# Kernel optimization log

Hardware: AMD Instinct MI355X
Metric: run time of the kernel (lower is better)

Reference implementation:

```python
import jax, jax.numpy as jnp
import numpy as np
from jax import lax

H = 32      # n_heads
D = 128     # head_dim
HID = 4096  # hidden_dim
CQ, CK, CH = 4, 9, 2
G = H // CH  # conv groups == groupnorm groups == 16


def setup_inputs() -> dict:
    key = jax.random.key(0)
    ks = jax.random.split(key, 8)
    q_seqlen = np.array([512, 384, 384, 256], dtype=np.int64)
    kv_seqlen = np.array([512, 384, 384, 256], dtype=np.int64)
    Sq = int(q_seqlen.sum())
    Sk = int(kv_seqlen.sum())
    x = jax.random.normal(ks[0], (Sq, HID), dtype=jnp.float32) * 0.02
    context = jax.random.normal(ks[1], (Sk, HID), dtype=jnp.float32) * 0.02
    wq = jax.random.normal(ks[2], (HID, H * D), dtype=jnp.float32) * 0.02
    wkv = jax.random.normal(ks[3], (HID, 2 * H * D), dtype=jnp.float32) * 0.02
    wo = jax.random.normal(ks[4], (H * D, HID), dtype=jnp.float32) * 0.02
    # grouped conv kernel [out=H, in_per_group=CH, CQ, CK]; dirac-like identity + noise
    conv_w = jax.random.normal(ks[5], (H, CH, CQ, CK), dtype=jnp.float32) * 0.05
    conv_w = conv_w.at[jnp.arange(H), jnp.arange(H) % CH, CQ // 2, CK // 2].add(1.0)
    gn_w = jnp.ones((H,), dtype=jnp.float32)
    gn_b = jnp.zeros((H,), dtype=jnp.float32)
    return {"x": x, "context": context, "wq": wq, "wkv": wkv, "wo": wo,
            "conv_w": conv_w, "gn_w": gn_w, "gn_b": gn_b,
            "q_seqlen": q_seqlen, "kv_seqlen": kv_seqlen}


def _block_diag_mask(q_seqlen, kv_seqlen, dtype):
    # block-diagonal ones mask for packed ragged sequences (static lengths)
    q_len = np.asarray(q_seqlen)
    k_len = np.asarray(kv_seqlen)
    seg_q = np.repeat(np.arange(len(q_len)), q_len)
    seg_k = np.repeat(np.arange(len(k_len)), k_len)
    return jnp.asarray(seg_q[:, None] == seg_k[None, :], dtype=dtype)


def reference(x, context, wq, wkv, wo, conv_w, gn_w, gn_b, q_seqlen, kv_seqlen):
    S = x.shape[0]
    mask = _block_diag_mask(q_seqlen, kv_seqlen, x.dtype)  # [Sq, Sk]
    scale = 1.0 / np.sqrt(D).astype(np.float32)
    q = (x @ wq).reshape(S, H, D).transpose(1, 0, 2) * scale        # [H, Sq, D]
    kv = context @ wkv
    k = kv[:, : H * D].reshape(-1, H, D).transpose(1, 0, 2)         # [H, Sk, D]
    v = kv[:, H * D :].reshape(-1, H, D).transpose(1, 0, 2)         # [H, Sk, D]
    attn = jnp.einsum('hqd,hkd->hqk', q, k) * mask[None]            # [H, Sq, Sk]
    # grouped Conv2d over (query, key) positions, channels = heads
    a = lax.conv_general_dilated(
        attn[None], conv_w, window_strides=(1, 1),
        padding=((CQ // 2, CQ // 2), (CK // 2, CK // 2)),
        dimension_numbers=('NCHW', 'OIHW', 'NCHW'),
        feature_group_count=G)[0]                                   # [H, Sq+1, Sk]
    a = a[:, :-1, :]  # c_q even -> drop extra row (c_k odd -> no col drop)
    a = jax.nn.softmax(a + mask[None], axis=-1)                     # note: +1 bias inside blocks, not -inf
    out = jnp.einsum('hqk,hkd->hqd', a, v)                          # [H, Sq, D]
    # GroupNorm(num_groups=G, channels=H) over [1, H, Sq, D]
    og = out.reshape(G, CH, S, D)
    mu = og.mean(axis=(1, 2, 3), keepdims=True)
    var = og.var(axis=(1, 2, 3), keepdims=True)
    og = (og - mu) * lax.rsqrt(var + 1e-5)
    out = og.reshape(H, S, D) * gn_w[:, None, None] + gn_b[:, None, None]
    out = out.transpose(1, 0, 2).reshape(S, H * D)
    return out @ wo
```

## Files before the change

kernel.cpp:

```cpp
#include <hip/hip_runtime.h>
#include <stdint.h>


#define H_   32
#define D_   128
#define HID_ 4096
#define WMAX2 944
#define LPAD 8

typedef unsigned short bfr;
typedef __attribute__((ext_vector_type(4))) float f32x4;
typedef __attribute__((ext_vector_type(4))) int   i32x4;
typedef __attribute__((ext_vector_type(8))) unsigned short u16x8;
typedef __attribute__((ext_vector_type(4))) unsigned short u16x4;

__device__ __forceinline__ bfr f2bf(float f) {
  uint32_t u = __float_as_uint(f);
  u += 0x7fffu + ((u >> 16) & 1u);
  return (bfr)(u >> 16);
}
__device__ __forceinline__ float bf2f(bfr u) {
  return __uint_as_float(((uint32_t)u) << 16);
}
__device__ __forceinline__ void mfma_bf16(f32x4& d, i32x4 a, i32x4 b) {
  asm volatile("v_mfma_f32_16x16x32_bf16 %0, %1, %2, %0" : "+v"(d) : "v"(a), "v"(b));
}
__device__ __forceinline__ void gload_lds16(const void* g, void* l) {
  __builtin_amdgcn_global_load_lds((__attribute__((address_space(1))) void*)g,
                                   (__attribute__((address_space(3))) void*)l,
                                   16, 0, 0);
}

__global__ __launch_bounds__(256) void seg_setup(
    const void* __restrict__ qsl, const void* __restrict__ ksl,
    int* __restrict__ segq, int* __restrict__ segk,
    int* __restrict__ bq, int* __restrict__ bk,
    float* __restrict__ stats, int S, int Sk, int nseg)
{
  __shared__ int sbq[16], sbk[16];
  const int tid = threadIdx.x;
  if (tid == 0) {
    {
      const int* q32 = (const int*)qsl;
      long long s32 = 0; bool ok32 = true;
      for (int i = 0; i < nseg; ++i) { int v = q32[i]; if (v < 1 || v > S) ok32 = false; s32 += v; }
      const bool use32 = ok32 && (s32 == S);
      const long long* q64 = (const long long*)qsl;
      sbq[0] = 0;
      for (int i = 0; i < nseg; ++i) sbq[i + 1] = sbq[i] + (use32 ? q32[i] : (int)q64[i]);
    }
    {
      const int* k32 = (const int*)ksl;
      long long s32 = 0; bool ok32 = true;
      for (int i = 0; i < nseg; ++i) { int v = k32[i]; if (v < 1 || v > Sk) ok32 = false; s32 += v; }
      const bool use32 = ok32 && (s32 == Sk);
      const long long* k64 = (const long long*)ksl;
      sbk[0] = 0;
      for (int i = 0; i < nseg; ++i) sbk[i + 1] = sbk[i] + (use32 ? k32[i] : (int)k64[i]);
    }
    for (int i = 0; i <= nseg; ++i) { bq[i] = sbq[i]; bk[i] = sbk[i]; }
  }
  if (tid < 32) stats[tid] = 0.f;
  __syncthreads();
  for (int i = tid; i < S; i += 256) {
    int s = 0;
    while (s < nseg - 1 && i >= sbq[s + 1]) ++s;
    segq[i] = s;
  }
  for (int i = tid; i < Sk; i += 256) {
    int s = 0;
    while (s < nseg - 1 && i >= sbk[s + 1]) ++s;
    segk[i] = s;
  }
}

__global__ __launch_bounds__(256) void cvt_bf16(
    const float* __restrict__ in, bfr* __restrict__ out, long long n)
{
  long long i = ((long long)blockIdx.x * 256 + threadIdx.x) * 8;
  if (i >= n) return;
  f32x4 a = *(const f32x4*)(in + i);
  f32x4 b = *(const f32x4*)(in + i + 4);
  u16x8 o;
  #pragma unroll
  for (int j = 0; j < 4; ++j) { o[j] = f2bf(a[j]); o[4 + j] = f2bf(b[j]); }
  *(u16x8*)(out + i) = o;
}

__global__ __launch_bounds__(256) void transpose_cvt(
    const float* __restrict__ in, bfr* __restrict__ out, int R, int ld)
{
  __shared__ float tile[64][65];
  const int t = threadIdx.x;
  const int rb = blockIdx.y * 64, cb = blockIdx.x * 64;
  const int row = t >> 2, c4 = (t & 3) * 16;
  const float* gp = in + (long long)(rb + row) * ld + cb + c4;
  #pragma unroll
  for (int j = 0; j < 4; ++j) {
    f32x4 v = *(const f32x4*)(gp + j * 4);
    #pragma unroll
    for (int q = 0; q < 4; ++q) tile[row][c4 + j * 4 + q] = v[q];
  }
  __syncthreads();
  const int cc = row, r4 = c4;
  u16x8 a, b;
  #pragma unroll
  for (int j = 0; j < 8; ++j) a[j] = f2bf(tile[r4 + j][cc]);
  #pragma unroll
  for (int j = 0; j < 8; ++j) b[j] = f2bf(tile[r4 + 8 + j][cc]);
  bfr* op = out + (long long)(cb + cc) * R + rb + r4;
  *(u16x8*)op = a;
  *(u16x8*)(op + 8) = b;
}

__global__ __launch_bounds__(256) void transpose_b16(
    const bfr* __restrict__ in, bfr* __restrict__ out, int R, int C)
{
  __shared__ bfr t[64][72];
  const int z = blockIdx.z;
  const bfr* ip = in + (long long)z * R * C;
  bfr* op = out + (long long)z * R * C;
  const int rb = blockIdx.y * 64, cb = blockIdx.x * 64;
  const int tr = threadIdx.x >> 3;
  const int tc = (threadIdx.x & 7) * 8;
  #pragma unroll
  for (int half = 0; half < 2; ++half) {
    const int r = tr + half * 32;
    u16x8 v = *(const u16x8*)(ip + (long long)(rb + r) * C + cb + tc);
    *(u16x8*)&t[r][tc] = v;
  }
  __syncthreads();
  #pragma unroll
  for (int half = 0; half < 2; ++half) {
    const int cc = tr + half * 32;
    u16x8 vv;
    #pragma unroll
    for (int j = 0; j < 8; ++j) vv[j] = t[tc + j][cc];
    *(u16x8*)(op + (long long)(cb + cc) * R + rb + tc) = vv;
  }
}

__global__ __launch_bounds__(256) void colsum_v(
    const bfr* __restrict__ vt, float* __restrict__ cs, int Sk)
{
  const int lane = threadIdx.x & 63, wave = threadIdx.x >> 6;
  const int row = blockIdx.x * 4 + wave;
  const bfr* src = vt + (long long)row * Sk;
  float s = 0.f;
  for (int i = lane * 8; i + 8 <= Sk; i += 512) {
    u16x8 v = *(const u16x8*)(src + i);
    #pragma unroll
    for (int j = 0; j < 8; ++j) s += bf2f(v[j]);
  }
  #pragma unroll
  for (int m = 1; m < 64; m <<= 1) s += __shfl_xor(s, m);
  if (lane == 0) cs[row] = s;
}

struct GemmAux {
  const int* segq; const int* segk; const int* bk;
  bfr* qb; bfr* kb; bfr* vrow;
  float* outb; float* stats;
  const float* fvArr; const float* colsum;
  float scale;
  int S, Sk, nOff;
};

enum { MODE_PLAIN = 0, MODE_Q = 1, MODE_KV = 2, MODE_QK = 3, MODE_PV = 4 };

template <int MODE, int KS = 1>
__global__ __launch_bounds__(256) void gemm_bt(
    const bfr* __restrict__ A, const bfr* __restrict__ Bt, void* __restrict__ Cout,
    int N, int K, int lda, int ldb,
    long long aZ, long long bZ, long long cZ, GemmAux aux)
{
  __shared__ bfr As[128 * 32];
  __shared__ bfr Bs[128 * 32];
  __shared__ float redS[8], redSS[8];
  const int tid = threadIdx.x;
  const int lane = tid & 63;
  const int wave = tid >> 6;
  const int z = blockIdx.z;

  int bx = blockIdx.x, by = blockIdx.y;
  {
    const int gx = gridDim.x, gy = gridDim.y;
    if (((gx & 3) == 0) && ((gy & 1) == 0)) {
      const int lid = by * gx + bx;
      const int xcd = lid & 7, inner = lid >> 3;
      const int cm = gy >> 1, cn = gx >> 2;
      by = (xcd >> 2) * cm + inner / cn;
      bx = (xcd & 3) * cn + inner % cn;
    }
  }
  const int m0 = by * 128;
  const int n0 = bx * 128;
  const bfr* Ap = A + (long long)z * aZ;
  const bfr* Bp = Bt + (long long)z * bZ;

  int kLo = 0, kHiV = K;
  if constexpr (KS > 1) { const int ksp = K / KS; kLo = z * ksp; kHiV = kLo + ksp; }
  if constexpr (MODE == MODE_PV) {
    const int t127 = min(m0 + 127, aux.S - 1);
    kLo = (max(aux.bk[aux.segq[max(m0 - 2, 0)]] - 4, 0)) & ~31;
    int th = min(aux.bk[aux.segq[min(t127 + 1, aux.S - 1)] + 1] + 4, aux.Sk);
    kHiV = min((th + 31) & ~31, aux.Sk);
  }

  const int wr = (wave >> 1) * 64;
  const int wc = (wave & 1) * 64;
  f32x4 acc[4][4];
  #pragma unroll
  for (int i = 0; i < 4; ++i)
    #pragma unroll
    for (int j = 0; j < 4; ++j) acc[i][j] = (f32x4){0.f, 0.f, 0.f, 0.f};

  const int srow = lane >> 2;
  const int scol = (((lane & 3) ^ ((lane >> 2) & 3)) << 3);
  const int rcol = (((lane >> 4) ^ (lane & 3)) << 3);

  const int kSteps = (kHiV - kLo) >> 5;
  for (int ks = 0; ks < kSteps; ++ks) {
    const int k0 = kLo + (ks << 5);
    #pragma unroll
    for (int c = 0; c < 4; ++c) {
      const int chunk = (wave << 2) + c;
      const int ci = chunk & 7;
      const int row = ci * 16 + srow;
      if (chunk < 8) gload_lds16(Ap + (long long)(m0 + row) * lda + k0 + scol, As + ci * 512);
      else           gload_lds16(Bp + (long long)(n0 + row) * ldb + k0 + scol, Bs + ci * 512);
    }
    __syncthreads();
    i32x4 af[4], bfv[4];
    #pragma unroll
    for (int i = 0; i < 4; ++i)
      af[i] = *(const i32x4*)&As[(wr + i * 16 + (lane & 15)) * 32 + rcol];
    #pragma unroll
    for (int i = 0; i < 4; ++i)
      bfv[i] = *(const i32x4*)&Bs[(wc + i * 16 + (lane & 15)) * 32 + rcol];
    #pragma unroll
    for (int i = 0; i < 4; ++i)
      #pragma unroll
      for (int j = 0; j < 4; ++j)
        mfma_bf16(acc[i][j], af[i], bfv[j]);
    __syncthreads();
  }

  float fvm[16], csn[4];
  if constexpr (MODE == MODE_PV) {
    #pragma unroll
    for (int i = 0; i < 4; ++i)
      #pragma unroll
      for (int r = 0; r < 4; ++r)
        fvm[i * 4 + r] = aux.fvArr[(long long)z * aux.S + m0 + wr + i * 16 + (lane >> 4) * 4 + r];
    #pragma unroll
    for (int j = 0; j < 4; ++j)
      csn[j] = aux.colsum[(long long)z * D_ + n0 + wc + j * 16 + (lane & 15)];
  }

  float sv = 0.f, sq2 = 0.f;
  #pragma unroll
  for (int i = 0; i < 4; ++i) {
    #pragma unroll
    for (int j = 0; j < 4; ++j) {
      #pragma unroll
      for (int r = 0; r < 4; ++r) {
        const int m = m0 + wr + i * 16 + (lane >> 4) * 4 + r;
        const int n = n0 + wc + j * 16 + (lane & 15);
        const float v = acc[i][j][r];
        if constexpr (KS > 1) {
          aux.outb[((long long)z * aux.S + m) * N + n] = v;
        } else if constexpr (MODE == MODE_PLAIN) {
          ((float*)Cout)[(long long)m * N + n] = v;
        } else if constexpr (MODE == MODE_Q) {
          const int hh = n >> 7, d = n & 127;
          aux.qb[((long long)hh * aux.S + m) * D_ + d] = f2bf(v * aux.scale);
        } else if constexpr (MODE == MODE_KV) {
          const int ng = n + aux.nOff;
          if (ng < H_ * D_) {
            const int hh = ng >> 7, d = ng & 127;
            aux.kb[((long long)hh * aux.Sk + m) * D_ + d] = f2bf(v);
          } else {
            const int nv = ng - H_ * D_;
            const int hh = nv >> 7, d = nv & 127;
            aux.vrow[((long long)hh * aux.Sk + m) * D_ + d] = f2bf(v);
          }
        } else if constexpr (MODE == MODE_PV) {
          const float vv = v + fvm[i * 4 + r] * csn[j];
          aux.outb[((long long)z * aux.S + m) * D_ + n] = vv;
          sv += vv; sq2 += vv * vv;
        }
      }
    }
  }

  if constexpr (MODE == MODE_PV && KS == 1) {
    #pragma unroll
    for (int msk = 1; msk < 64; msk <<= 1) {
      sv  += __shfl_xor(sv, msk);
      sq2 += __shfl_xor(sq2, msk);
    }
    if (lane == 0) { redS[wave] = sv; redSS[wave] = sq2; }
    __syncthreads();
    if (tid == 0) {
      const float a = redS[0] + redS[1] + redS[2] + redS[3];
      const float b = redSS[0] + redSS[1] + redSS[2] + redSS[3];
      atomicAdd(&aux.stats[(z >> 1) * 2 + 0], a);
      atomicAdd(&aux.stats[(z >> 1) * 2 + 1], b);
    }
  }
}

__global__ __launch_bounds__(256) void gemm_qk(
    const bfr* __restrict__ A, const bfr* __restrict__ Bt, bfr* __restrict__ Cout,
    long long aZ, long long bZ, long long cZ, GemmAux aux)
{
  __shared__ bfr As[128 * 128];
  __shared__ bfr Bs[128 * 128];
  const int tid = threadIdx.x;
  const int lane = tid & 63;
  const int wave = tid >> 6;
  const int z = blockIdx.z;
  const int m0 = blockIdx.y * 128;
  const int n0 = blockIdx.x * 128;

  const int t127 = min(m0 + 127, aux.S - 1);
  const int loT = max(aux.bk[aux.segq[max(m0 - 2, 0)]] - 4, 0);
  const int hiT = min(aux.bk[aux.segq[min(t127 + 1, aux.S - 1)] + 1] + 4, aux.Sk);
  if (n0 > hiT + 16 || n0 + 127 < loT - 16) return;
  const int sm0 = aux.segq[m0], sm1 = aux.segq[t127];
  const int sn0 = aux.segk[n0], sn1 = aux.segk[min(n0 + 127, aux.Sk - 1)];
  if (sm1 < sn0 || sn1 < sm0) {
    bfr* C = Cout + (long long)z * cZ + (long long)m0 * aux.Sk + n0;
    const i32x4 zz = {0, 0, 0, 0};
    #pragma unroll
    for (int c = 0; c < 8; ++c) {
      int id = c * 256 + tid;
      int r = id >> 4, col = (id & 15) * 8;
      *(i32x4*)(C + (long long)r * aux.Sk + col) = zz;
    }
    return;
  }

  const bfr* Ap = A + (long long)z * aZ;
  const bfr* Bp = Bt + (long long)z * bZ;

  const int srow = lane >> 4;
  const int scol = (lane & 15) * 8;
  #pragma unroll
  for (int c = 0; c < 16; ++c) {
    const int chunk = wave * 16 + c;
    if (chunk < 32) {
      const int r = chunk * 4 + srow;
      gload_lds16(Ap + (long long)(m0 + r) * D_ + scol, As + chunk * 512);
    } else {
      const int r = (chunk - 32) * 4 + srow;
      gload_lds16(Bp + (long long)(n0 + r) * D_ + scol, Bs + (chunk - 32) * 512);
    }
  }
  __syncthreads();

  const int wr = (wave >> 1) * 64;
  const int wc = (wave & 1) * 64;
  f32x4 acc[4][4];
  #pragma unroll
  for (int i = 0; i < 4; ++i)
    #pragma unroll
    for (int j = 0; j < 4; ++j) acc[i][j] = (f32x4){0.f, 0.f, 0.f, 0.f};

  #pragma unroll
  for (int ks = 0; ks < 4; ++ks) {
    const int colb = ks * 32 + (lane >> 4) * 8;
    i32x4 af[4], bfv[4];
    #pragma unroll
    for (int i = 0; i < 4; ++i)
      af[i] = *(const i32x4*)&As[(wr + i * 16 + (lane & 15)) * 128 + colb];
    #pragma unroll
    for (int j = 0; j < 4; ++j)
      bfv[j] = *(const i32x4*)&Bs[(wc + j * 16 + (lane & 15)) * 128 + colb];
    #pragma unroll
    for (int i = 0; i < 4; ++i)
      #pragma unroll
      for (int j = 0; j < 4; ++j)
        mfma_bf16(acc[i][j], af[i], bfv[j]);
  }

  const bool qkUni = (sm0 == sm1) && (sn0 == sn1);
  int sgm[16], sgn[4];
  if (!qkUni) {
    #pragma unroll
    for (int i = 0; i < 4; ++i)
      #pragma unroll
      for (int r = 0; r < 4; ++r)
        sgm[i * 4 + r] = aux.segq[m0 + wr + i * 16 + (lane >> 4) * 4 + r];
    #pragma unroll
    for (int j = 0; j < 4; ++j) sgn[j] = aux.segk[n0 + wc + j * 16 + (lane & 15)];
  }
  #pragma unroll
  for (int i = 0; i < 4; ++i) {
    #pragma unroll
    for (int j = 0; j < 4; ++j) {
      #pragma unroll
      for (int r = 0; r < 4; ++r) {
        const int m = m0 + wr + i * 16 + (lane >> 4) * 4 + r;
        const int n = n0 + wc + j * 16 + (lane & 15);
        const float v = acc[i][j][r];
        const float vv = (qkUni || sgm[i * 4 + r] == sgn[j]) ? v : 0.f;
        Cout[(long long)z * cZ + (long long)m * aux.Sk + n] = f2bf(vv);
      }
    }
  }
}

__global__ __launch_bounds__(256) void reduce_split_q(
    const float* __restrict__ part, bfr* __restrict__ qb, float scale, int S)
{
  const long long MN = (long long)S * HID_;
  const long long i = ((long long)blockIdx.x * 256 + threadIdx.x) * 8;
  if (i >= MN) return;
  const f32x4 a0 = *(const f32x4*)(part + i);
  const f32x4 a1 = *(const f32x4*)(part + i + 4);
  const f32x4 b0 = *(const f32x4*)(part + MN + i);
  const f32x4 b1 = *(const f32x4*)(part + MN + i + 4);
  const int m = (int)(i >> 12);
  const int n = (int)(i & 4095);
  const int hh = n >> 7, d = n & 127;
  u16x8 o;
  #pragma unroll
  for (int j = 0; j < 4; ++j) {
    o[j]     = f2bf((a0[j] + b0[j]) * scale);
    o[4 + j] = f2bf((a1[j] + b1[j]) * scale);
  }
  *(u16x8*)(qb + ((long long)hh * S + m) * D_ + d) = o;
}

__global__ __launch_bounds__(256) void reduce_split_f32(
    const float* __restrict__ part, float* __restrict__ out, long long MN)
{
  const long long i = ((long long)blockIdx.x * 256 + threadIdx.x) * 8;
  if (i >= MN) return;
  const f32x4 a0 = *(const f32x4*)(part + i);
  const f32x4 a1 = *(const f32x4*)(part + i + 4);
  const f32x4 b0 = *(const f32x4*)(part + MN + i);
  const f32x4 b1 = *(const f32x4*)(part + MN + i + 4);
  f32x4 o0, o1;
  #pragma unroll
  for (int j = 0; j < 4; ++j) { o0[j] = a0[j] + b0[j]; o1[j] = a1[j] + b1[j]; }
  *(f32x4*)(out + i) = o0;
  *(f32x4*)(out + i + 4) = o1;
}

__global__ __launch_bounds__(512) void conv_softmax5(
    const bfr* __restrict__ attn, const float* __restrict__ conv_w,
    bfr* __restrict__ p, float* __restrict__ fvArr,
    const int* __restrict__ segq, const int* __restrict__ segk,
    const int* __restrict__ bk, int S, int Sk, int h0)
{
  __shared__ float wsh[144];
  __shared__ bfr sIn[11][WMAX2];
  const int tid = threadIdx.x, lane = tid & 63, w = tid >> 6;
  const int q0 = blockIdx.x * 8;
  const int c0 = blockIdx.y * 2;
  const int h  = h0 + c0;
  if (tid < 144) wsh[tid] = conv_w[h * 72 + tid];

  const int lo0 = (max(bk[segq[max(q0 - 2, 0)]] - 4, 0)) & ~7;
  const int hiL = min(bk[segq[min(q0 + 8, S - 1)] + 1] + 4, Sk);
  const int g0 = max(lo0 - 8, 0) & ~7;
  const int g1 = min(hiL + 4, Sk);
  const int W8 = (g1 - g0 + 7) >> 3;

  const int qa = q0 + w;
  const int loA = (max(bk[segq[max(qa - 2, 0)]] - 4, 0)) & ~7;
  const int hiA = min(bk[segq[min(qa + 1, S - 1)] + 1] + 4, Sk);
  const int sqA = segq[qa];
  const int width = hiA - loA;

  float lg[2][4][4];
  #pragma unroll
  for (int e = 0; e < 2; ++e)
    #pragma unroll
    for (int pp = 0; pp < 4; ++pp)
      #pragma unroll
      for (int o = 0; o < 4; ++o) lg[e][pp][o] = 0.f;

  if (tid < 11) {
    const u16x8 zz8 = {0,0,0,0,0,0,0,0};
    *(u16x8*)&sIn[tid][0] = zz8;
    *(u16x8*)&sIn[tid][LPAD + W8 * 8] = zz8;
  }

  for (int pass = 0; pass < 2; ++pass) {
    if (pass) __syncthreads();
    const bfr* src0 = attn + (long long)(c0 + pass) * S * Sk;
    for (int it = tid; it < 11 * 116; it += 512) {
      const int ri = it / 116;
      const int j  = it - ri * 116;
      if (j < W8) {
        const int r = q0 - 2 + ri;
        u16x8 v = {0,0,0,0,0,0,0,0};
        if (r >= 0 && r < S) v = *(const u16x8*)(src0 + (long long)r * Sk + g0 + j * 8);
        *(u16x8*)&sIn[ri][LPAD + j * 8] = v;
      }
    }
    __syncthreads();

    #pragma unroll
    for (int pp = 0; pp < 4; ++pp) {
      const int kk = loA + pp * 256 + lane * 4;
      if (kk < hiA) {
        const int ib = LPAD + kk - 4 - g0;
        #pragma unroll
        for (int rr = 0; rr < 4; ++rr) {
          const bfr* sp = &sIn[w + rr][ib];
          u16x4 u0 = *(const u16x4*)(sp);
          u16x4 u1 = *(const u16x4*)(sp + 4);
          u16x4 u2 = *(const u16x4*)(sp + 8);
          float xx[12];
          #pragma unroll
          for (int j2 = 0; j2 < 4; ++j2) {
            xx[j2]     = bf2f(u0[j2]);
            xx[4 + j2] = bf2f(u1[j2]);
            xx[8 + j2] = bf2f(u2[j2]);
          }
          const float* wv0 = &wsh[(pass * 4 + rr) * 9];
          const float* wv1 = wv0 + 72;
          #pragma unroll
          for (int dk = 0; dk < 9; ++dk) {
            #pragma unroll
            for (int o = 0; o < 4; ++o) {
              lg[0][pp][o] += xx[o + dk] * wv0[dk];
              lg[1][pp][o] += xx[o + dk] * wv1[dk];
            }
          }
        }
      }
    }
  }

  float lmax0 = -1e30f, lmax1 = -1e30f;
  #pragma unroll
  for (int pp = 0; pp < 4; ++pp) {
    const int kk = loA + pp * 256 + lane * 4;
    i32x4 sk4 = {0, 0, 0, 0};
    if (kk < Sk) sk4 = *(const i32x4*)&segk[kk];
    #pragma unroll
    for (int o = 0; o < 4; ++o) {
      const int k = kk + o;
      float v0 = -1e30f, v1 = -1e30f;
      if (k < hiA) {
        const float mb = (sk4[o] == sqA) ? 1.f : 0.f;
        v0 = lg[0][pp][o] + mb; lmax0 = fmaxf(lmax0, v0);
        v1 = lg[1][pp][o] + mb; lmax1 = fmaxf(lmax1, v1);
      }
      lg[0][pp][o] = v0; lg[1][pp][o] = v1;
    }
  }
  #pragma unroll
  for (int m = 1; m < 64; m <<= 1) {
    lmax0 = fmaxf(lmax0, __shfl_xor(lmax0, m));
    lmax1 = fmaxf(lmax1, __shfl_xor(lmax1, m));
  }
  const float M0 = fmaxf(lmax0, 0.f), M1 = fmaxf(lmax1, 0.f);
  float ls0 = 0.f, ls1 = 0.f;
  #pragma unroll
  for (int pp = 0; pp < 4; ++pp)
    #pragma unroll
    for (int o = 0; o < 4; ++o) {
      const float e0 = __expf(lg[0][pp][o] - M0);
      const float e1 = __expf(lg[1][pp][o] - M1);
      lg[0][pp][o] = e0; ls0 += e0;
      lg[1][pp][o] = e1; ls1 += e1;
    }
  #pragma unroll
  for (int m = 1; m < 64; m <<= 1) {
    ls0 += __shfl_xor(ls0, m);
    ls1 += __shfl_xor(ls1, m);
  }
  const float eo0 = __expf(-M0), eo1 = __expf(-M1);
  const float iv0 = 1.f / (ls0 + (float)(Sk - width) * eo0);
  const float iv1 = 1.f / (ls1 + (float)(Sk - width) * eo1);
  const float fv0 = eo0 * iv0, fv1 = eo1 * iv1;

  const int t0 = (q0 >> 7) << 7;
  const int t127 = min(t0 + 127, S - 1);
  const int tLo = (max(bk[segq[max(t0 - 2, 0)]] - 4, 0)) & ~31;
  int tHi = min(bk[segq[min(t127 + 1, S - 1)] + 1] + 4, Sk);
  tHi = min((tHi + 31) & ~31, Sk);

  bfr* row0 = p + ((long long)(c0 + 0) * S + qa) * Sk;
  bfr* row1 = p + ((long long)(c0 + 1) * S + qa) * Sk;
  #pragma unroll
  for (int pp = 0; pp < 4; ++pp) {
    const int kk = loA + pp * 256 + lane * 4;
    if (kk + 3 < hiA) {
      u16x4 s0, s1;
      #pragma unroll
      for (int o = 0; o < 4; ++o) {
        s0[o] = f2bf(lg[0][pp][o] * iv0 - fv0);
        s1[o] = f2bf(lg[1][pp][o] * iv1 - fv1);
      }
      *(u16x4*)(row0 + kk) = s0;
      *(u16x4*)(row1 + kk) = s1;
    } else if (kk < hiA) {
      for (int o = 0; o < 4; ++o)
        if (kk + o < hiA) {
          row0[kk + o] = f2bf(lg[0][pp][o] * iv0 - fv0);
          row1[kk + o] = f2bf(lg[1][pp][o] * iv1 - fv1);
        }
    }
  }
  const u16x4 z4 = {0, 0, 0, 0};
  for (int k = tLo + lane * 4; k < loA; k += 256) {
    *(u16x4*)(row0 + k) = z4;
    *(u16x4*)(row1 + k) = z4;
  }
  for (int k = hiA + lane; k < tHi; k += 64) { row0[k] = 0; row1[k] = 0; }
  if (lane == 0) {
    fvArr[(long long)(h + 0) * S + qa] = fv0;
    fvArr[(long long)(h + 1) * S + qa] = fv1;
  }
}

__global__ void gn_finalize(const float* __restrict__ stats, float* __restrict__ mr, float invcnt)
{
  const int g = threadIdx.x;
  if (g < 16) {
    const float s = stats[2 * g], ss = stats[2 * g + 1];
    const float mu = s * invcnt;
    const float var = ss * invcnt - mu * mu;
    mr[2 * g] = mu;
    mr[2 * g + 1] = rsqrtf(var + 1e-5f);
  }
}

__global__ __launch_bounds__(256) void gn_apply(
    const float* __restrict__ outb, const float* __restrict__ mr,
    const float* __restrict__ gnw, const float* __restrict__ gnb,
    bfr* __restrict__ y, int S)
{
  const int h = blockIdx.y;
  const long long inner = ((long long)blockIdx.x * 256 + threadIdx.x) * 8;
  if (inner >= (long long)S * D_) return;
  const int s = (int)(inner >> 7), d = (int)(inner & 127);
  const int g = h >> 1;
  const float mu = mr[2 * g], rs = mr[2 * g + 1];
  const float wgt = gnw[h] * rs;
  const float b = gnb[h] - mu * wgt;
  const float* src = outb + (long long)h * S * D_ + inner;
  const f32x4 a = *(const f32x4*)(src);
  const f32x4 c = *(const f32x4*)(src + 4);
  u16x8 o;
  #pragma unroll
  for (int j = 0; j < 4; ++j) { o[j] = f2bf(a[j] * wgt + b); o[4 + j] = f2bf(c[j] * wgt + b); }
  *(u16x8*)(y + (long long)s * HID_ + h * D_ + d) = o;
}

extern "C" void kernel_launch(void* const* d_in, const int* in_sizes, int n_in,
                              void* d_out, int out_size, void* d_ws, size_t ws_size,
                              hipStream_t stream)
{
  const float* x      = (const float*)d_in[0];
  const float* ctx    = (const float*)d_in[1];
  const float* wq     = (const float*)d_in[2];
  const float* wkv    = (const float*)d_in[3];
  const float* wo     = (const float*)d_in[4];
  const float* conv_w = (const float*)d_in[5];
  const float* gnw    = (const float*)d_in[6];
  const float* gnb    = (const float*)d_in[7];
  const void*  qsl    = d_in[8];
  const void*  ksl    = d_in[9];
  const int S    = in_sizes[0] / HID_;
  const int Sk   = in_sizes[1] / HID_;
  const int nseg = in_sizes[8];

  auto al = [](size_t v) { return (v + 255) & ~(size_t)255; };
  char* base = (char*)d_ws;
  size_t off = 0;
  auto take = [&](size_t bytes) -> char* { char* r = base + off; off += al(bytes); return r; };

  int*   segq  = (int*)take((size_t)S * 4);
  int*   segk  = (int*)take((size_t)Sk * 4);
  int*   bq    = (int*)take(64);
  int*   bk    = (int*)take(64);
  float* stats = (float*)take(128);
  float* mr    = (float*)take(128);
  float* fvArr = (float*)take((size_t)H_ * S * 4);
  float* csV   = (float*)take((size_t)H_ * D_ * 4);
  bfr*   qb    = (bfr*)take((size_t)H_ * S * D_ * 2);
  bfr*   kbuf  = (bfr*)take((size_t)H_ * Sk * D_ * 2);
  bfr*   vrow  = (bfr*)take((size_t)H_ * Sk * D_ * 2);
  bfr*   vt    = (bfr*)take((size_t)H_ * Sk * D_ * 2);
  float* outb  = (float*)take((size_t)H_ * S * D_ * 4);
  const size_t poolBase = off;
  char*  pool  = base + poolBase;

  const int Smax = (S > Sk) ? S : Sk;
  const size_t A1 = al((size_t)Smax * HID_ * 2);
  const size_t WT = al((size_t)HID_ * HID_ * 2);
  const size_t PART = al((size_t)2 * S * HID_ * 4);

  const size_t CAmin = al((size_t)4 * S * Sk * 2);
  const size_t fusedNeed = (A1 + 2 * WT > 2 * CAmin) ? (A1 + 2 * WT) : (2 * CAmin);
  const bool fused = (poolBase + fusedNeed <= ws_size);
  const bool splitOK = (poolBase + A1 + 2 * WT + PART <= ws_size);
  const size_t wNeed = A1 + (fused ? 2 : 1) * WT + (splitOK ? PART : 0);

  int nc = 4;
  {
    const int cands[3] = {32, 16, 8};
    for (int ci = 0; ci < 3; ++ci) {
      const size_t CA = al((size_t)cands[ci] * S * Sk * 2);
      const size_t need = (wNeed > 2 * CA) ? wNeed : (2 * CA);
      if (poolBase + need <= ws_size) { nc = cands[ci]; break; }
    }
  }
  const size_t CA = al((size_t)nc * S * Sk * 2);
  bfr*   xcb    = (bfr*)pool;
  bfr*   wT     = (bfr*)(pool + A1);
  float* partB  = (float*)(pool + A1 + 2 * WT);
  bfr*   attn_c = (bfr*)pool;
  bfr*   pbuf_c = (bfr*)(pool + CA);

  seg_setup<<<1, 256, 0, stream>>>(qsl, ksl, segq, segk, bq, bk, stats, S, Sk, nseg);

  GemmAux aux{};
  aux.segq = segq; aux.segk = segk; aux.bk = bk;
  aux.qb = qb; aux.kb = kbuf; aux.vrow = vrow;
  aux.outb = outb; aux.stats = stats;
  aux.fvArr = fvArr; aux.colsum = csV;
  aux.scale = 0.08838834764831845f;
  aux.S = S; aux.Sk = Sk; aux.nOff = 0;

  const long long MN = (long long)S * HID_;
  const int nRed = (int)((MN / 8 + 255) / 256);

  const long long nx = (long long)S * HID_;
  cvt_bf16<<<(int)((nx / 8 + 255) / 256), 256, 0, stream>>>(x, xcb, nx);
  transpose_cvt<<<dim3(HID_ / 64, HID_ / 64), 256, 0, stream>>>(wq, wT, HID_, HID_);
  if (splitOK) {
    GemmAux auxQ = aux; auxQ.outb = partB;
    gemm_bt<MODE_Q, 2><<<dim3(HID_ / 128, S / 128, 2), 256, 0, stream>>>(
        xcb, wT, nullptr, HID_, HID_, HID_, HID_, 0, 0, 0, auxQ);
    reduce_split_q<<<nRed, 256, 0, stream>>>(partB, qb, aux.scale, S);
  } else {
    gemm_bt<MODE_Q><<<dim3(HID_ / 128, S / 128, 1), 256, 0, stream>>>(
        xcb, wT, nullptr, HID_, HID_, HID_, HID_, 0, 0, 0, aux);
  }

  const long long nctx = (long long)Sk * HID_;
  cvt_bf16<<<(int)((nctx / 8 + 255) / 256), 256, 0, stream>>>(ctx, xcb, nctx);
  if (fused) {
    transpose_cvt<<<dim3(2 * HID_ / 64, HID_ / 64), 256, 0, stream>>>(wkv, wT, HID_, 2 * HID_);
    gemm_bt<MODE_KV><<<dim3(2 * HID_ / 128, Sk / 128, 1), 256, 0, stream>>>(
        xcb, wT, nullptr, 2 * HID_, HID_, HID_, HID_, 0, 0, 0, aux);
  } else {
    transpose_cvt<<<dim3(HID_ / 64, HID_ / 64), 256, 0, stream>>>(wkv, wT, HID_, 2 * HID_);
    gemm_bt<MODE_KV><<<dim3(HID_ / 128, Sk / 128, 1), 256, 0, stream>>>(
        xcb, wT, nullptr, HID_, HID_, HID_, HID_, 0, 0, 0, aux);
    transpose_cvt<<<dim3(HID_ / 64, HID_ / 64), 256, 0, stream>>>(wkv + HID_, wT, HID_, 2 * HID_);
    GemmAux auxV = aux; auxV.nOff = H_ * D_;
    gemm_bt<MODE_KV><<<dim3(HID_ / 128, Sk / 128, 1), 256, 0, stream>>>(
        xcb, wT, nullptr, HID_, HID_, HID_, HID_, 0, 0, 0, auxV);
  }

  transpose_b16<<<dim3(D_ / 64, Sk / 64, H_), 256, 0, stream>>>(vrow, vt, Sk, D_);
  colsum_v<<<H_ * D_ / 4, 256, 0, stream>>>(vt, csV, Sk);

  for (int h0 = 0; h0 < H_; h0 += nc) {
    gemm_qk<<<dim3(Sk / 128, S / 128, nc), 256, 0, stream>>>(
        qb + (size_t)h0 * S * D_, kbuf + (size_t)h0 * Sk * D_, attn_c,
        (long long)S * D_, (long long)Sk * D_, (long long)S * Sk, aux);
    conv_softmax5<<<dim3(S / 8, nc / 2), 512, 0, stream>>>(
        attn_c, conv_w, pbuf_c, fvArr, segq, segk, bk, S, Sk, h0);
    GemmAux auxP = aux;
    auxP.outb = outb + (size_t)h0 * S * D_;
    auxP.stats = stats + h0;
    auxP.fvArr = fvArr + (size_t)h0 * S;
    auxP.colsum = csV + (size_t)h0 * D_;
    gemm_bt<MODE_PV><<<dim3(1, S / 128, nc), 256, 0, stream>>>(
        pbuf_c, vt + (size_t)h0 * D_ * Sk, nullptr,
        D_, Sk, Sk, Sk,
        (long long)S * Sk, (long long)D_ * Sk, 0, auxP);
  }

  gn_finalize<<<1, 32, 0, stream>>>(stats, mr, 1.0f / (2.0f * S * D_));
  gn_apply<<<dim3((S * D_) / 2048, H_), 256, 0, stream>>>(outb, mr, gnw, gnb, xcb, S);
  transpose_cvt<<<dim3(HID_ / 64, HID_ / 64), 256, 0, stream>>>(wo, wT, HID_, HID_);
  if (splitOK) {
    GemmAux auxO = aux; auxO.outb = partB;
    gemm_bt<MODE_PLAIN, 2><<<dim3(HID_ / 128, S / 128, 2), 256, 0, stream>>>(
        xcb, wT, nullptr, HID_, HID_, HID_, HID_, 0, 0, 0, auxO);
    reduce_split_f32<<<nRed, 256, 0, stream>>>(partB, (float*)d_out, MN);
  } else {
    gemm_bt<MODE_PLAIN><<<dim3(HID_ / 128, S / 128, 1), 256, 0, stream>>>(
        xcb, wT, d_out, HID_, HID_, HID_, HID_, 0, 0, 0, aux);
  }
}
```

Measured before the change: 540.4 us.

## Double-buffer GEMM LDS tiles, swizzle QK LDS layout, widen conv-softmax to 8 columns

The main GEMM now keeps two LDS buffers and prefetches the next K-slab while the current one feeds the MFMAs. The old pair of full __syncthreads per step becomes a partial vmcnt wait plus raw barriers. The QK kernel's LDS staging gets an XOR swizzle on the column index to cut bank conflicts on fragment reads, and the GEMM's swizzle pattern is changed too. The conv-softmax kernel makes each lane handle 8 contiguous keys instead of 4, using wider loads and stores. The risks are higher register pressure and whether the vmcnt(4) count is correct for the async LDS loads.

```diff
diff --git a/kernel.cpp b/kernel.cpp
--- a/kernel.cpp
+++ b/kernel.cpp
@@ -174,8 +174,8 @@
     int N, int K, int lda, int ldb,
     long long aZ, long long bZ, long long cZ, GemmAux aux)
 {
-  __shared__ bfr As[128 * 32];
-  __shared__ bfr Bs[128 * 32];
+  __shared__ bfr As[2][128 * 32];
+  __shared__ bfr Bs[2][128 * 32];
   __shared__ float redS[8], redSS[8];
   const int tid = threadIdx.x;
   const int lane = tid & 63;
@@ -216,34 +216,47 @@
     for (int j = 0; j < 4; ++j) acc[i][j] = (f32x4){0.f, 0.f, 0.f, 0.f};
 
   const int srow = lane >> 2;
-  const int scol = (((lane & 3) ^ ((lane >> 2) & 3)) << 3);
-  const int rcol = (((lane >> 4) ^ (lane & 3)) << 3);
-
-  const int kSteps = (kHiV - kLo) >> 5;
-  for (int ks = 0; ks < kSteps; ++ks) {
-    const int k0 = kLo + (ks << 5);
+  const int scol = (((lane & 3) ^ ((lane >> 3) & 3)) << 3);
+  const int rcol = (((lane >> 4) ^ ((lane >> 1) & 3)) << 3);
+
+  auto STAGE = [&](int k0, int b) {
     #pragma unroll
     for (int c = 0; c < 4; ++c) {
       const int chunk = (wave << 2) + c;
       const int ci = chunk & 7;
       const int row = ci * 16 + srow;
-      if (chunk < 8) gload_lds16(Ap + (long long)(m0 + row) * lda + k0 + scol, As + ci * 512);
-      else           gload_lds16(Bp + (long long)(n0 + row) * ldb + k0 + scol, Bs + ci * 512);
-    }
-    __syncthreads();
+      if (chunk < 8) gload_lds16(Ap + (long long)(m0 + row) * lda + k0 + scol, &As[b][ci * 512]);
+      else           gload_lds16(Bp + (long long)(n0 + row) * ldb + k0 + scol, &Bs[b][ci * 512]);
+    }
+  };
+
+  const int kSteps = (kHiV - kLo) >> 5;
+  STAGE(kLo, 0);
+  int cur = 0;
+  for (int t = 0; t < kSteps; ++t) {
+    if (t + 1 < kSteps) {
+      STAGE(kLo + ((t + 1) << 5), cur ^ 1);
+      asm volatile("s_waitcnt vmcnt(4)" ::: "memory");
+    } else {
+      asm volatile("s_waitcnt vmcnt(0)" ::: "memory");
+    }
+    __builtin_amdgcn_s_barrier();
+    __builtin_amdgcn_sched_barrier(0);
     i32x4 af[4], bfv[4];
     #pragma unroll
     for (int i = 0; i < 4; ++i)
-      af[i] = *(const i32x4*)&As[(wr + i * 16 + (lane & 15)) * 32 + rcol];
+      af[i] = *(const i32x4*)&As[cur][(wr + i * 16 + (lane & 15)) * 32 + rcol];
     #pragma unroll
     for (int i = 0; i < 4; ++i)
-      bfv[i] = *(const i32x4*)&Bs[(wc + i * 16 + (lane & 15)) * 32 + rcol];
+      bfv[i] = *(const i32x4*)&Bs[cur][(wc + i * 16 + (lane & 15)) * 32 + rcol];
     #pragma unroll
     for (int i = 0; i < 4; ++i)
       #pragma unroll
       for (int j = 0; j < 4; ++j)
         mfma_bf16(acc[i][j], af[i], bfv[j]);
-    __syncthreads();
+    __builtin_amdgcn_sched_barrier(0);
+    __builtin_amdgcn_s_barrier();
+    cur ^= 1;
   }
 
   float fvm[16], csn[4];
@@ -346,17 +359,15 @@
   const bfr* Bp = Bt + (long long)z * bZ;
 
   const int srow = lane >> 4;
-  const int scol = (lane & 15) * 8;
   #pragma unroll
   for (int c = 0; c < 16; ++c) {
     const int chunk = wave * 16 + c;
-    if (chunk < 32) {
-      const int r = chunk * 4 + srow;
-      gload_lds16(Ap + (long long)(m0 + r) * D_ + scol, As + chunk * 512);
-    } else {
-      const int r = (chunk - 32) * 4 + srow;
-      gload_lds16(Bp + (long long)(n0 + r) * D_ + scol, Bs + (chunk - 32) * 512);
-    }
+    const int cl = chunk & 31;
+    const int f = (2 * cl + (lane >> 5)) & 7;
+    const int sc = ((lane & 15) ^ f) * 8;
+    const int r = cl * 4 + srow;
+    if (chunk < 32) gload_lds16(Ap + (long long)(m0 + r) * D_ + sc, As + cl * 512);
+    else            gload_lds16(Bp + (long long)(n0 + r) * D_ + sc, Bs + cl * 512);
   }
   __syncthreads();
 
@@ -368,9 +379,11 @@
     #pragma unroll
     for (int j = 0; j < 4; ++j) acc[i][j] = (f32x4){0.f, 0.f, 0.f, 0.f};
 
+  const int rf = (lane >> 1) & 7;
   #pragma unroll
   for (int ks = 0; ks < 4; ++ks) {
-    const int colb = ks * 32 + (lane >> 4) * 8;
+    const int slot = (4 * ks + (lane >> 4)) ^ rf;
+    const int colb = slot * 8;
     i32x4 af[4], bfv[4];
     #pragma unroll
     for (int i = 0; i < 4; ++i)
@@ -450,7 +463,7 @@
   *(f32x4*)(out + i + 4) = o1;
 }
 
-__global__ __launch_bounds__(512) void conv_softmax5(
+__global__ __launch_bounds__(512) void conv_softmax6(
     const bfr* __restrict__ attn, const float* __restrict__ conv_w,
     bfr* __restrict__ p, float* __restrict__ fvArr,
     const int* __restrict__ segq, const int* __restrict__ segk,
@@ -476,13 +489,13 @@
   const int sqA = segq[qa];
   const int width = hiA - loA;
 
-  float lg[2][4][4];
+  float lg[2][2][8];
   #pragma unroll
   for (int e = 0; e < 2; ++e)
     #pragma unroll
-    for (int pp = 0; pp < 4; ++pp)
-      #pragma unroll
-      for (int o = 0; o < 4; ++o) lg[e][pp][o] = 0.f;
+    for (int pp = 0; pp < 2; ++pp)
+      #pragma unroll
+      for (int o = 0; o < 8; ++o) lg[e][pp][o] = 0.f;
 
   if (tid < 11) {
     const u16x8 zz8 = {0,0,0,0,0,0,0,0};
@@ -506,8 +519,8 @@
     __syncthreads();
 
     #pragma unroll
-    for (int pp = 0; pp < 4; ++pp) {
-      const int kk = loA + pp * 256 + lane * 4;
+    for (int pp = 0; pp < 2; ++pp) {
+      const int kk = loA + pp * 512 + lane * 8;
       if (kk < hiA) {
         const int ib = LPAD + kk - 4 - g0;
         #pragma unroll
@@ -516,19 +529,21 @@
           u16x4 u0 = *(const u16x4*)(sp);
           u16x4 u1 = *(const u16x4*)(sp + 4);
           u16x4 u2 = *(const u16x4*)(sp + 8);
-          float xx[12];
+          u16x4 u3 = *(const u16x4*)(sp + 12);
+          float xx[16];
           #pragma unroll
           for (int j2 = 0; j2 < 4; ++j2) {
-            xx[j2]     = bf2f(u0[j2]);
-            xx[4 + j2] = bf2f(u1[j2]);
-            xx[8 + j2] = bf2f(u2[j2]);
+            xx[j2]      = bf2f(u0[j2]);
+            xx[4 + j2]  = bf2f(u1[j2]);
+            xx[8 + j2]  = bf2f(u2[j2]);
+            xx[12 + j2] = bf2f(u3[j2]);
           }
           const float* wv0 = &wsh[(pass * 4 + rr) * 9];
           const float* wv1 = wv0 + 72;
           #pragma unroll
           for (int dk = 0; dk < 9; ++dk) {
             #pragma unroll
-            for (int o = 0; o < 4; ++o) {
+            for (int o = 0; o < 8; ++o) {
               lg[0][pp][o] += xx[o + dk] * wv0[dk];
               lg[1][pp][o] += xx[o + dk] * wv1[dk];
             }
@@ -540,16 +555,24 @@
 
   float lmax0 = -1e30f, lmax1 = -1e30f;
   #pragma unroll
-  for (int pp = 0; pp < 4; ++pp) {
-    const int kk = loA + pp * 256 + lane * 4;
-    i32x4 sk4 = {0, 0, 0, 0};
-    if (kk < Sk) sk4 = *(const i32x4*)&segk[kk];
-    #pragma unroll
-    for (int o = 0; o < 4; ++o) {
+  for (int pp = 0; pp < 2; ++pp) {
+    const int kk = loA + pp * 512 + lane * 8;
+    int sk8[8];
+    if (kk < Sk) {
+      i32x4 a = *(const i32x4*)&segk[kk];
+      i32x4 b = *(const i32x4*)&segk[kk + 4];
+      #pragma unroll
+      for (int j = 0; j < 4; ++j) { sk8[j] = a[j]; sk8[4 + j] = b[j]; }
+    } else {
+      #pragma unroll
+      for (int j = 0; j < 8; ++j) sk8[j] = -1;
+    }
+    #pragma unroll
+    for (int o = 0; o < 8; ++o) {
       const int k = kk + o;
       float v0 = -1e30f, v1 = -1e30f;
       if (k < hiA) {
-        const float mb = (sk4[o] == sqA) ? 1.f : 0.f;
+        const float mb = (sk8[o] == sqA) ? 1.f : 0.f;
         v0 = lg[0][pp][o] + mb; lmax0 = fmaxf(lmax0, v0);
         v1 = lg[1][pp][o] + mb; lmax1 = fmaxf(lmax1, v1);
       }
@@ -564,9 +587,9 @@
   const float M0 = fmaxf(lmax0, 0.f), M1 = fmaxf(lmax1, 0.f);
   float ls0 = 0.f, ls1 = 0.f;
   #pragma unroll
-  for (int pp = 0; pp < 4; ++pp)
-    #pragma unroll
-    for (int o = 0; o < 4; ++o) {
+  for (int pp = 0; pp < 2; ++pp)
+    #pragma unroll
+    for (int o = 0; o < 8; ++o) {
       const float e0 = __expf(lg[0][pp][o] - M0);
       const float e1 = __expf(lg[1][pp][o] - M1);
       lg[0][pp][o] = e0; ls0 += e0;
@@ -591,19 +614,19 @@
   bfr* row0 = p + ((long long)(c0 + 0) * S + qa) * Sk;
   bfr* row1 = p + ((long long)(c0 + 1) * S + qa) * Sk;
   #pragma unroll
-  for (int pp = 0; pp < 4; ++pp) {
-    const int kk = loA + pp * 256 + lane * 4;
-    if (kk + 3 < hiA) {
-      u16x4 s0, s1;
-      #pragma unroll
-      for (int o = 0; o < 4; ++o) {
+  for (int pp = 0; pp < 2; ++pp) {
+    const int kk = loA + pp * 512 + lane * 8;
+    if (kk + 7 < hiA) {
+      u16x8 s0, s1;
+      #pragma unroll
+      for (int o = 0; o < 8; ++o) {
         s0[o] = f2bf(lg[0][pp][o] * iv0 - fv0);
         s1[o] = f2bf(lg[1][pp][o] * iv1 - fv1);
       }
-      *(u16x4*)(row0 + kk) = s0;
-      *(u16x4*)(row1 + kk) = s1;
+      *(u16x8*)(row0 + kk) = s0;
+      *(u16x8*)(row1 + kk) = s1;
     } else if (kk < hiA) {
-      for (int o = 0; o < 4; ++o)
+      for (int o = 0; o < 8; ++o)
         if (kk + o < hiA) {
           row0[kk + o] = f2bf(lg[0][pp][o] * iv0 - fv0);
           row1[kk + o] = f2bf(lg[1][pp][o] * iv1 - fv1);
@@ -771,7 +794,7 @@
     gemm_qk<<<dim3(Sk / 128, S / 128, nc), 256, 0, stream>>>(
         qb + (size_t)h0 * S * D_, kbuf + (size_t)h0 * Sk * D_, attn_c,
         (long long)S * D_, (long long)Sk * D_, (long long)S * Sk, aux);
-    conv_softmax5<<<dim3(S / 8, nc / 2), 512, 0, stream>>>(
+    conv_softmax6<<<dim3(S / 8, nc / 2), 512, 0, stream>>>(
         attn_c, conv_w, pbuf_c, fvArr, segq, segk, bk, S, Sk, h0);
     GemmAux auxP = aux;
     auxP.outb = outb + (size_t)h0 * S * D_;
```

After: 550.2 us. Within noise of the previous version (+1.8%).
